# Performance work log

Hardware: AMD Instinct MI355X
Metric: run time of the kernel (lower is better)

The kernel has to match this reference:

```python
import jax, jax.numpy as jnp
import numpy as np

NUM_HEADS = 12

def setup_inputs() -> dict:
    key = jax.random.key(0)
    k1, k2, k3 = jax.random.split(key, 3)
    B, T, H = 2, 2048, 768
    x = jax.random.normal(k1, (B, T, H), dtype=jnp.float32)
    attn_mask = jnp.ones((B, T), dtype=jnp.int32)
    Wqkv = jax.random.normal(k2, (H, 3 * H), dtype=jnp.float32) * 0.02
    bqkv = jnp.zeros((3 * H,), dtype=jnp.float32)
    Wproj = jax.random.normal(k3, (H, H), dtype=jnp.float32) * 0.02
    bproj = jnp.zeros((H,), dtype=jnp.float32)
    return {"x": x, "attn_mask": attn_mask, "Wqkv": Wqkv, "bqkv": bqkv,
            "Wproj": Wproj, "bproj": bproj}

def reference(x, attn_mask, Wqkv, bqkv, Wproj, bproj):
    B, T, H = x.shape
    nh = NUM_HEADS
    hd = H // nh
    qkv = x @ Wqkv + bqkv                      # [B,T,3H]
    q, k, v = jnp.split(qkv, 3, axis=-1)
    # [B,T,H] -> [B,nh,T,hd]
    def heads(t):
        return t.reshape(B, T, nh, hd).transpose(0, 2, 1, 3)
    q, k, v = heads(q), heads(k), heads(v)
    scores = jnp.einsum('bhqd,bhkd->bhqk', q, k) / jnp.sqrt(jnp.float32(hd))
    causal = jnp.tril(jnp.ones((T, T), dtype=bool))          # allowed positions
    key_ok = attn_mask.astype(bool)[:, None, None, :]        # [B,1,1,T]
    allowed = causal[None, None] & key_ok
    scores = jnp.where(allowed, scores, -jnp.inf)
    weights = jax.nn.softmax(scores, axis=-1)                # dropout=0 (eval)
    out = jnp.einsum('bhqk,bhkd->bhqd', weights, v)
    out = out.transpose(0, 2, 1, 3).reshape(B, T, H)
    return out @ Wproj + bproj
```

## Files before the change

kernel.cpp:

```cpp
#include <hip/hip_runtime.h>
#include <stdint.h>

typedef unsigned short u16;
typedef unsigned int   u32;
typedef unsigned char  u8;
typedef __attribute__((ext_vector_type(8))) short short8;
typedef __attribute__((ext_vector_type(4))) float f32x4;
typedef __attribute__((ext_vector_type(4))) unsigned short u16x4;
typedef __attribute__((ext_vector_type(4))) unsigned int u32x4;

#define DEV static __device__ __forceinline__

static constexpr int Bc = 2, Tc = 2048, Hc = 768, NH = 12, HD = 64;
static constexpr int BTc = Bc * Tc;
static constexpr int N3 = 3 * Hc;
static constexpr int NBH = Bc * NH;
static constexpr int NITEMS = 32 * NBH;
static constexpr float QSCALE = 0.125f * 1.44269504088896f;
static constexpr float MRINIT = -1.0e38f;
static constexpr float SMASK  = -3.0e38f;

DEV u16 f2bf(float f) {
  u32 u = __float_as_uint(f);
  u32 r = (u + 0x7fffu + ((u >> 16) & 1u)) >> 16;
  return (u16)r;
}

DEV float fexp2(float x) {
#if __has_builtin(__builtin_amdgcn_exp2f)
  return __builtin_amdgcn_exp2f(x);
#else
  return exp2f(x);
#endif
}

DEV u32 cvtpk_bf16(float lo, float hi) {
  u32 r;
  asm("v_cvt_pk_bf16_f32 %0, %1, %2" : "=v"(r) : "v"(lo), "v"(hi));
  return r;
}

DEV void gl_lds16(const u16* g, u16* l) {
  __builtin_amdgcn_global_load_lds(
      (const __attribute__((address_space(1))) u32*)g,
      (__attribute__((address_space(3))) u32*)l, 16, 0, 0);
}

#define MFMA(a, b, c) __builtin_amdgcn_mfma_f32_16x16x32_bf16((a), (b), (c), 0, 0, 0)

__global__ void k_cvt(const float4* __restrict__ in, uint4* __restrict__ out, int n8,
                      const int* __restrict__ mask, u8* __restrict__ flags,
                      u32* __restrict__ ctr) {
  if (blockIdx.x == 0 && threadIdx.x < 64) {
    int t = threadIdx.x;
    if (t == 0) *ctr = 0;
    int b = t >> 5, kb = t & 31;
    const int* m = mask + b * Tc + kb * 64;
    int all = 1;
    for (int i = 0; i < 64; ++i) all &= (m[i] != 0);
    flags[b * 32 + kb] = (u8)all;
  }
  int i = blockIdx.x * 256 + threadIdx.x;
  if (i >= n8) return;
  float4 a = in[2 * i], b = in[2 * i + 1];
  uint4 o;
  o.x = f2bf(a.x) | ((u32)f2bf(a.y) << 16);
  o.y = f2bf(a.z) | ((u32)f2bf(a.w) << 16);
  o.z = f2bf(b.x) | ((u32)f2bf(b.y) << 16);
  o.w = f2bf(b.z) | ((u32)f2bf(b.w) << 16);
  out[i] = o;
}

__global__ __launch_bounds__(256) void k_transpose_w2(const float* __restrict__ Wqkv,
                                                      const float* __restrict__ Wproj,
                                                      u16* __restrict__ WqkvT,
                                                      u16* __restrict__ WprojT) {
  __shared__ u16 tile[64][65];
  int y = blockIdx.y, x = blockIdx.x;
  const float* in; u16* out; int R, C, r0, c0;
  if (y < 12) { in = Wqkv; out = WqkvT; R = Hc; C = N3; r0 = y * 64; c0 = x * 64; }
  else {
    if (x >= 12) return;
    in = Wproj; out = WprojT; R = Hc; C = Hc; r0 = (y - 12) * 64; c0 = x * 64;
  }
  int tx = threadIdx.x, ty = threadIdx.y;
  for (int i = ty; i < 64; i += 4)
    tile[i][tx] = f2bf(in[(size_t)(r0 + i) * C + c0 + tx]);
  __syncthreads();
  for (int i = ty; i < 64; i += 4)
    out[(size_t)(c0 + i) * R + r0 + tx] = tile[tx][i];
}

template <int EPI>
__global__ __launch_bounds__(256) void k_gemm(const u16* __restrict__ A,
                                              const u16* __restrict__ BTm,
                                              const float* __restrict__ bias,
                                              u16* __restrict__ oQ, u16* __restrict__ oK,
                                              u16* __restrict__ oV, float* __restrict__ oF,
                                              int M, int N, int K) {
  __shared__ u16 As[3][4096];
  __shared__ u16 Bs[3][4096];
  const int tid = threadIdx.x;
  const int lane = tid & 63, wave = tid >> 6;
  const int wr = wave >> 1, wc = wave & 1;

  const int gx = gridDim.x;
  const int nwg = gx * gridDim.y;
  const int lin = blockIdx.y * gx + blockIdx.x;
  const int wg = (lin & 7) * (nwg >> 3) + (lin >> 3);
  const int row0 = (wg / gx) * 128, col0 = (wg % gx) * 128;

  f32x4 acc[4][4];
#pragma unroll
  for (int m = 0; m < 4; ++m)
#pragma unroll
    for (int n = 0; n < 4; ++n) acc[m][n] = (f32x4)(0.f);

  const int srow = lane >> 2;
  const int sg = lane & 3;
  const int sf = (lane >> 3) & 3;
  const int kfetch = ((sg ^ sf) * 8);

  const int r16 = lane & 15;
  const int g = lane >> 4;
  const int fr = (r16 >> 1) & 3;
  const int koff = ((g ^ fr) * 8);

  auto stageG = [&](int slot, int k0) {
#pragma unroll
    for (int p = 0; p < 2; ++p) {
      int seg = wave * 2 + p;
      int row = seg * 16 + srow;
      gl_lds16(A + (size_t)(row0 + row) * K + k0 + kfetch, &As[slot][seg * 512 + lane * 8]);
      gl_lds16(BTm + (size_t)(col0 + row) * K + k0 + kfetch, &Bs[slot][seg * 512 + lane * 8]);
    }
  };

  const int nk = K >> 5;
  stageG(0, 0);
  if (nk > 1) stageG(1, 32);

  for (int kt = 0; kt < nk; ++kt) {
    if (kt + 1 < nk) asm volatile("s_waitcnt vmcnt(4)" ::: "memory");
    else             asm volatile("s_waitcnt vmcnt(0)" ::: "memory");
    __builtin_amdgcn_sched_barrier(0);
    __builtin_amdgcn_s_barrier();
    __builtin_amdgcn_sched_barrier(0);
    if (kt + 2 < nk) stageG((kt + 2) % 3, (kt + 2) * 32);

    const u16* Ac = &As[kt % 3][0];
    const u16* Bcur = &Bs[kt % 3][0];
    short8 af[4], bf[4];
#pragma unroll
    for (int m = 0; m < 4; ++m)
      af[m] = *(const short8*)&Ac[(wr * 64 + m * 16 + r16) * 32 + koff];
#pragma unroll
    for (int n = 0; n < 4; ++n)
      bf[n] = *(const short8*)&Bcur[(wc * 64 + n * 16 + r16) * 32 + koff];
#pragma unroll
    for (int m = 0; m < 4; ++m)
#pragma unroll
      for (int n = 0; n < 4; ++n)
        acc[m][n] = MFMA(af[m], bf[n], acc[m][n]);
  }

#pragma unroll
  for (int m = 0; m < 4; ++m) {
    int rowg = row0 + wr * 64 + m * 16 + g * 4;
#pragma unroll
    for (int n = 0; n < 4; ++n) {
      int colg = col0 + wc * 64 + n * 16 + r16;
      float bv = bias[colg];
      if constexpr (EPI == 0) {
        int which = colg / Hc;
        int hc = colg - which * Hc;
        int h = hc >> 6, d = hc & 63;
        int b = rowg >> 11, t0 = rowg & 2047;
        if (which == 2) {
          int o = t0 & 31;
          int t0p = (t0 & ~31) | (((o >> 2) & 3) * 8 + ((o >> 4) & 1) * 4);
          u16x4 pk;
#pragma unroll
          for (int r = 0; r < 4; ++r) pk[r] = f2bf(acc[m][n][r] + bv);
          *(u16x4*)&oV[((size_t)(b * NH + h) * HD + d) * Tc + t0p] = pk;
        } else {
#pragma unroll
          for (int r = 0; r < 4; ++r) {
            float v = acc[m][n][r] + bv;
            size_t dst = ((size_t)(b * NH + h) * Tc + t0 + r) * HD + d;
            if (which == 0) oQ[dst] = f2bf(v * QSCALE);
            else            oK[dst] = f2bf(v);
          }
        }
      } else {
#pragma unroll
        for (int r = 0; r < 4; ++r)
          oF[(size_t)(rowg + r) * Hc + colg] = acc[m][n][r] + bv;
      }
    }
  }
}

__global__ __launch_bounds__(512, 4) void k_attn(const u16* __restrict__ Qh,
                                                 const u16* __restrict__ Kh,
                                                 const u16* __restrict__ VT,
                                                 const int* __restrict__ mask,
                                                 const u8* __restrict__ flags,
                                                 u16* __restrict__ O,
                                                 u32* __restrict__ ctr) {
  __shared__ u16 Ks[2][4096];
  __shared__ u16 Vs[2][4096];
  __shared__ float mlb[128];
  __shared__ int s_item;
  const int tid = threadIdx.x, lane = tid & 63, wave = tid >> 6;
  const int qgrp = wave >> 1;
  const int kh = wave & 1;
  const int r16 = lane & 15, g = lane >> 4;
  const int r7 = r16 & 7;
  const int skey = lane >> 3;
  const int sgr = lane & 7;
  const int sgd = ((sgr ^ skey) * 8);

  const int off0 = r16 * 64 + ((g ^ r7) * 8);
  const int off1 = r16 * 64 + (((4 + g) ^ r7) * 8);
  const int offv = kh ? off1 : off0;

  for (;;) {
    if (tid == 0) s_item = (int)atomicAdd(ctr, 1u);
    __syncthreads();
    const int item = s_item;
    if (item >= NITEMS) break;
    const int qt = 31 - item / NBH;
    const int bh = item % NBH;
    const int b = bh / NH, h = bh - b * NH;
    const int q0 = qt * 64;
    const int nt = qt + 1;
    const int qg = q0 + qgrp * 16 + r16;
    const int* mrow = mask + b * Tc;
    const u8* frow = flags + b * 32;

    const u16* qbase = Qh + ((size_t)bh * Tc + qg) * HD;
    const short8 qf0 = *(const short8*)(qbase + g * 8);
    const short8 qf1 = *(const short8*)(qbase + 32 + g * 8);

    f32x4 acc[4];
#pragma unroll
    for (int n = 0; n < 4; ++n) acc[n] = (f32x4)(0.f);
    float mrun = MRINIT, lrun = 0.f;

    const u16* kgb = Kh + (size_t)bh * Tc * HD;
    const u16* vgb = VT + (size_t)bh * HD * Tc;

    auto stage = [&](int slot, int kb) {
      int rloc = wave * 8 + skey;
      gl_lds16(kgb + (size_t)(kb + rloc) * HD + sgd, &Ks[slot][wave * 512 + lane * 8]);
      gl_lds16(vgb + (size_t)rloc * Tc + kb + sgd, &Vs[slot][wave * 512 + lane * 8]);
    };

    stage(0, 0);

    for (int t = 0; t < nt; ++t) {
      const int kb = t * 64;

      asm volatile("s_waitcnt vmcnt(0)" ::: "memory");
      __builtin_amdgcn_sched_barrier(0);
      __builtin_amdgcn_s_barrier();
      __builtin_amdgcn_sched_barrier(0);

      if (t + 1 < nt) stage((t + 1) & 1, kb + 64);

      const u16* Kc = &Ks[t & 1][0];
      const u16* Vc = &Vs[t & 1][0];

      f32x4 s0, s1;
      {
        const int ng = 2 * kh;
        short8 kf0 = *(const short8*)&Kc[ng * 1024 + off0];
        short8 kf1 = *(const short8*)&Kc[ng * 1024 + off1];
        f32x4 z = (f32x4)(0.f);
        z = MFMA(kf0, qf0, z); z = MFMA(kf1, qf1, z);
        s0 = z;
        short8 kf2 = *(const short8*)&Kc[(ng + 1) * 1024 + off0];
        short8 kf3 = *(const short8*)&Kc[(ng + 1) * 1024 + off1];
        f32x4 w = (f32x4)(0.f);
        w = MFMA(kf2, qf0, w); w = MFMA(kf3, qf1, w);
        s1 = w;
      }

      const int kbw = kb + 32 * kh;
      const bool diag = (t == nt - 1);
      if (diag || !frow[t]) {
        const int fl = frow[t];
#pragma unroll
        for (int np = 0; np < 2; ++np)
#pragma unroll
          for (int r = 0; r < 4; ++r) {
            int keyg = kbw + 16 * np + 4 * g + r;
            bool ok = fl ? true : (mrow[keyg] != 0);
            if (diag) ok = ok && (keyg <= qg);
            if (!ok) { if (np == 0) s0[r] = SMASK; else s1[r] = SMASK; }
          }
      }

      float lm = fmaxf(fmaxf(fmaxf(s0[0], s0[1]), fmaxf(s0[2], s0[3])),
                       fmaxf(fmaxf(s1[0], s1[1]), fmaxf(s1[2], s1[3])));
      if (!__all(lm <= mrun + 8.0f)) {
        float rm = fmaxf(lm, __shfl_xor(lm, 16));
        rm = fmaxf(rm, __shfl_xor(rm, 32));
        float nm = fmaxf(mrun, rm);
        float alpha = fexp2(mrun - nm);
        mrun = nm;
        lrun *= alpha;
#pragma unroll
        for (int r = 0; r < 4; ++r) {
          float ar = __shfl(alpha, g * 4 + r);
          acc[0][r] *= ar; acc[1][r] *= ar; acc[2][r] *= ar; acc[3][r] *= ar;
        }
      }
      float p0[4], p1[4];
#pragma unroll
      for (int r = 0; r < 4; ++r) {
        p0[r] = fexp2(s0[r] - mrun);
        p1[r] = fexp2(s1[r] - mrun);
      }
      lrun += ((p0[0] + p0[1]) + (p0[2] + p0[3])) + ((p1[0] + p1[1]) + (p1[2] + p1[3]));

      u32x4 PL;
      PL[0] = cvtpk_bf16(p0[0], p0[1]); PL[1] = cvtpk_bf16(p0[2], p0[3]);
      PL[2] = cvtpk_bf16(p1[0], p1[1]); PL[3] = cvtpk_bf16(p1[2], p1[3]);
      short8 pa = __builtin_bit_cast(short8, PL);
#pragma unroll
      for (int n = 0; n < 4; ++n) {
        short8 vf = *(const short8*)&Vc[n * 1024 + offv];
        acc[n] = MFMA(pa, vf, acc[n]);
      }
      __builtin_amdgcn_sched_barrier(0);
    }

    float lt = lrun + __shfl_xor(lrun, 16);
    lt += __shfl_xor(lt, 32);

    __syncthreads();
    float* ab = (float*)&Ks[0][0] + qgrp * 1024;
    if (kh == 1) {
#pragma unroll
      for (int n = 0; n < 4; ++n)
#pragma unroll
        for (int r = 0; r < 4; ++r)
          ab[(4 * g + r) * 64 + 16 * n + r16] = acc[n][r];
      if (g == 0) {
        mlb[qgrp * 32 + r16 * 2]     = mrun;
        mlb[qgrp * 32 + r16 * 2 + 1] = lt;
      }
    }
    __syncthreads();
    if (kh == 0) {
#pragma unroll
      for (int r = 0; r < 4; ++r) {
        int q = 4 * g + r;
        float mA = __shfl(mrun, q);
        float lA = __shfl(lt, q);
        float mB = mlb[qgrp * 32 + q * 2];
        float lB = mlb[qgrp * 32 + q * 2 + 1];
        float ms = fmaxf(mA, mB);
        float cA = fexp2(mA - ms);
        float cB = fexp2(mB - ms);
        float linv = 1.0f / (lA * cA + lB * cB);
        int qr = q0 + qgrp * 16 + q;
        u16* orow = O + ((size_t)(b * Tc + qr)) * Hc + h * 64;
#pragma unroll
        for (int n = 0; n < 4; ++n) {
          float v = (acc[n][r] * cA + ab[q * 64 + 16 * n + r16] * cB) * linv;
          orow[n * 16 + r16] = f2bf(v);
        }
      }
    }
  }
}

extern "C" void kernel_launch(void* const* d_in, const int* in_sizes, int n_in,
                              void* d_out, int out_size, void* d_ws, size_t ws_size,
                              hipStream_t stream) {
  const float* x = (const float*)d_in[0];
  const int* mask = (const int*)d_in[1];
  const float* Wqkv = (const float*)d_in[2];
  const float* bqkv = (const float*)d_in[3];
  const float* Wproj = (const float*)d_in[4];
  const float* bproj = (const float*)d_in[5];
  float* out = (float*)d_out;

  char* ws = (char*)d_ws;
  size_t off = 0;
  auto alloc = [&](size_t bytes) {
    char* p = ws + off;
    off += (bytes + 255) & ~(size_t)255;
    return p;
  };
  u16* xb     = (u16*)alloc((size_t)BTc * Hc * 2);
  u16* WqkvT  = (u16*)alloc((size_t)N3 * Hc * 2);
  u16* WprojT = (u16*)alloc((size_t)Hc * Hc * 2);
  u16* Qh     = (u16*)alloc((size_t)BTc * Hc * 2);
  u16* Kh     = (u16*)alloc((size_t)BTc * Hc * 2);
  u16* VT     = (u16*)alloc((size_t)BTc * Hc * 2);
  u32* ctr    = (u32*)alloc(256);
  u8*  flags  = (u8*)alloc(256);
  u16* Ob     = xb;

  int n8 = BTc * Hc / 8;
  k_cvt<<<(n8 + 255) / 256, 256, 0, stream>>>((const float4*)x, (uint4*)xb, n8,
                                              mask, flags, ctr);
  k_transpose_w2<<<dim3(36, 24), dim3(64, 4), 0, stream>>>(Wqkv, Wproj, WqkvT, WprojT);
  k_gemm<0><<<dim3(N3 / 128, BTc / 128), 256, 0, stream>>>(xb, WqkvT, bqkv, Qh, Kh, VT,
                                                           nullptr, BTc, N3, Hc);
  k_attn<<<dim3(NITEMS), 512, 0, stream>>>(Qh, Kh, VT, mask, flags, Ob, ctr);
  k_gemm<1><<<dim3(Hc / 128, BTc / 128), 256, 0, stream>>>(Ob, WprojT, bproj, nullptr,
                                                           nullptr, nullptr, out, BTc, Hc, Hc);
}
```

Before: 106.7 us.

## Load K/V fragments directly from global, partition attention work per XCD, merge prep kernels

The attention kernel stops staging K and V tiles into LDS through a double-buffered global-to-LDS pipeline with barriers. Each wave now reads its MFMA fragments straight from global memory and relies on cache reuse. Work items are split into per-XCD queues, each with its own atomic counter and three batch-head pairs, so a head's K/V stays in one XCD's L2. The kernel adds s_setprio around the MFMA sections, and the launch is cut to 512 persistent blocks. The cast and transpose prep kernels are merged into one launch. The change risks exposing global-load latency and uncoalesced reads in exchange for removing per-tile barriers.

```diff
diff --git a/kernel.cpp b/kernel.cpp
--- a/kernel.cpp
+++ b/kernel.cpp
@@ -15,7 +15,7 @@
 static constexpr int BTc = Bc * Tc;
 static constexpr int N3 = 3 * Hc;
 static constexpr int NBH = Bc * NH;
-static constexpr int NITEMS = 32 * NBH;
+static constexpr int IPX = 96;
 static constexpr float QSCALE = 0.125f * 1.44269504088896f;
 static constexpr float MRINIT = -1.0e38f;
 static constexpr float SMASK  = -3.0e38f;
@@ -48,47 +48,51 @@
 
 #define MFMA(a, b, c) __builtin_amdgcn_mfma_f32_16x16x32_bf16((a), (b), (c), 0, 0, 0)
 
-__global__ void k_cvt(const float4* __restrict__ in, uint4* __restrict__ out, int n8,
-                      const int* __restrict__ mask, u8* __restrict__ flags,
-                      u32* __restrict__ ctr) {
-  if (blockIdx.x == 0 && threadIdx.x < 64) {
-    int t = threadIdx.x;
-    if (t == 0) *ctr = 0;
-    int b = t >> 5, kb = t & 31;
+__global__ __launch_bounds__(256) void k_prep(const float* __restrict__ x,
+                                              const float* __restrict__ Wqkv,
+                                              const float* __restrict__ Wproj,
+                                              u16* __restrict__ xb,
+                                              u16* __restrict__ WqkvT,
+                                              u16* __restrict__ WprojT,
+                                              const int* __restrict__ mask,
+                                              u8* __restrict__ flags,
+                                              u32* __restrict__ ctr) {
+  const int bid = blockIdx.x, tid = threadIdx.x;
+  if (bid == 0 && tid < 64) {
+    if (tid < 8) ctr[tid] = 0;
+    int b = tid >> 5, kb = tid & 31;
     const int* m = mask + b * Tc + kb * 64;
     int all = 1;
     for (int i = 0; i < 64; ++i) all &= (m[i] != 0);
     flags[b * 32 + kb] = (u8)all;
   }
-  int i = blockIdx.x * 256 + threadIdx.x;
-  if (i >= n8) return;
-  float4 a = in[2 * i], b = in[2 * i + 1];
-  uint4 o;
-  o.x = f2bf(a.x) | ((u32)f2bf(a.y) << 16);
-  o.y = f2bf(a.z) | ((u32)f2bf(a.w) << 16);
-  o.z = f2bf(b.x) | ((u32)f2bf(b.y) << 16);
-  o.w = f2bf(b.z) | ((u32)f2bf(b.w) << 16);
-  out[i] = o;
-}
-
-__global__ __launch_bounds__(256) void k_transpose_w2(const float* __restrict__ Wqkv,
-                                                      const float* __restrict__ Wproj,
-                                                      u16* __restrict__ WqkvT,
-                                                      u16* __restrict__ WprojT) {
-  __shared__ u16 tile[64][65];
-  int y = blockIdx.y, x = blockIdx.x;
-  const float* in; u16* out; int R, C, r0, c0;
-  if (y < 12) { in = Wqkv; out = WqkvT; R = Hc; C = N3; r0 = y * 64; c0 = x * 64; }
-  else {
-    if (x >= 12) return;
-    in = Wproj; out = WprojT; R = Hc; C = Hc; r0 = (y - 12) * 64; c0 = x * 64;
+  if (bid < 864) {
+    __shared__ u16 tile[64][65];
+    int xg = bid % 36, y = bid / 36;
+    const float* in; u16* out; int R, C, r0, c0;
+    if (y < 12) { in = Wqkv; out = WqkvT; R = Hc; C = N3; r0 = y * 64; c0 = xg * 64; }
+    else {
+      if (xg >= 12) return;
+      in = Wproj; out = WprojT; R = Hc; C = Hc; r0 = (y - 12) * 64; c0 = xg * 64;
+    }
+    int tx = tid & 63, ty = tid >> 6;
+    for (int i = ty; i < 64; i += 4)
+      tile[i][tx] = f2bf(in[(size_t)(r0 + i) * C + c0 + tx]);
+    __syncthreads();
+    for (int i = ty; i < 64; i += 4)
+      out[(size_t)(c0 + i) * R + r0 + tx] = tile[tx][i];
+  } else {
+    int i = (bid - 864) * 256 + tid;
+    if (i >= BTc * Hc / 8) return;
+    const float4* in4 = (const float4*)x;
+    float4 a = in4[2 * i], b = in4[2 * i + 1];
+    uint4 o;
+    o.x = f2bf(a.x) | ((u32)f2bf(a.y) << 16);
+    o.y = f2bf(a.z) | ((u32)f2bf(a.w) << 16);
+    o.z = f2bf(b.x) | ((u32)f2bf(b.y) << 16);
+    o.w = f2bf(b.z) | ((u32)f2bf(b.w) << 16);
+    ((uint4*)xb)[i] = o;
   }
-  int tx = threadIdx.x, ty = threadIdx.y;
-  for (int i = ty; i < 64; i += 4)
-    tile[i][tx] = f2bf(in[(size_t)(r0 + i) * C + c0 + tx]);
-  __syncthreads();
-  for (int i = ty; i < 64; i += 4)
-    out[(size_t)(c0 + i) * R + r0 + tx] = tile[tx][i];
 }
 
 template <int EPI>
@@ -208,30 +212,23 @@
                                                  const u8* __restrict__ flags,
                                                  u16* __restrict__ O,
                                                  u32* __restrict__ ctr) {
-  __shared__ u16 Ks[2][4096];
-  __shared__ u16 Vs[2][4096];
+  __shared__ float ab[4][1024];
   __shared__ float mlb[128];
   __shared__ int s_item;
   const int tid = threadIdx.x, lane = tid & 63, wave = tid >> 6;
   const int qgrp = wave >> 1;
   const int kh = wave & 1;
   const int r16 = lane & 15, g = lane >> 4;
-  const int r7 = r16 & 7;
-  const int skey = lane >> 3;
-  const int sgr = lane & 7;
-  const int sgd = ((sgr ^ skey) * 8);
-
-  const int off0 = r16 * 64 + ((g ^ r7) * 8);
-  const int off1 = r16 * 64 + (((4 + g) ^ r7) * 8);
-  const int offv = kh ? off1 : off0;
+
+  const int xcd = blockIdx.x & 7;
 
   for (;;) {
-    if (tid == 0) s_item = (int)atomicAdd(ctr, 1u);
+    if (tid == 0) s_item = (int)atomicAdd(ctr + xcd, 1u);
     __syncthreads();
     const int item = s_item;
-    if (item >= NITEMS) break;
-    const int qt = 31 - item / NBH;
-    const int bh = item % NBH;
+    if (item >= IPX) break;
+    const int qt = 31 - item / 3;
+    const int bh = xcd * 3 + item % 3;
     const int b = bh / NH, h = bh - b * NH;
     const int q0 = qt * 64;
     const int nt = qt + 1;
@@ -248,46 +245,31 @@
     for (int n = 0; n < 4; ++n) acc[n] = (f32x4)(0.f);
     float mrun = MRINIT, lrun = 0.f;
 
-    const u16* kgb = Kh + (size_t)bh * Tc * HD;
-    const u16* vgb = VT + (size_t)bh * HD * Tc;
-
-    auto stage = [&](int slot, int kb) {
-      int rloc = wave * 8 + skey;
-      gl_lds16(kgb + (size_t)(kb + rloc) * HD + sgd, &Ks[slot][wave * 512 + lane * 8]);
-      gl_lds16(vgb + (size_t)rloc * Tc + kb + sgd, &Vs[slot][wave * 512 + lane * 8]);
-    };
-
-    stage(0, 0);
+    const u16* kp = Kh + (size_t)bh * Tc * HD + (size_t)(32 * kh + r16) * HD + 8 * g;
+    const u16* vp = VT + (size_t)bh * HD * Tc + (size_t)r16 * Tc + 32 * kh + 8 * g;
 
     for (int t = 0; t < nt; ++t) {
       const int kb = t * 64;
-
-      asm volatile("s_waitcnt vmcnt(0)" ::: "memory");
-      __builtin_amdgcn_sched_barrier(0);
-      __builtin_amdgcn_s_barrier();
-      __builtin_amdgcn_sched_barrier(0);
-
-      if (t + 1 < nt) stage((t + 1) & 1, kb + 64);
-
-      const u16* Kc = &Ks[t & 1][0];
-      const u16* Vc = &Vs[t & 1][0];
+      const int kbw = kb + 32 * kh;
+
+      const u16* kt0 = kp + (size_t)kb * HD;
+      short8 kf0 = *(const short8*)(kt0);
+      short8 kf1 = *(const short8*)(kt0 + 32);
+      short8 kf2 = *(const short8*)(kt0 + 1024);
+      short8 kf3 = *(const short8*)(kt0 + 1024 + 32);
 
       f32x4 s0, s1;
+      __builtin_amdgcn_s_setprio(1);
       {
-        const int ng = 2 * kh;
-        short8 kf0 = *(const short8*)&Kc[ng * 1024 + off0];
-        short8 kf1 = *(const short8*)&Kc[ng * 1024 + off1];
         f32x4 z = (f32x4)(0.f);
         z = MFMA(kf0, qf0, z); z = MFMA(kf1, qf1, z);
         s0 = z;
-        short8 kf2 = *(const short8*)&Kc[(ng + 1) * 1024 + off0];
-        short8 kf3 = *(const short8*)&Kc[(ng + 1) * 1024 + off1];
         f32x4 w = (f32x4)(0.f);
         w = MFMA(kf2, qf0, w); w = MFMA(kf3, qf1, w);
         s1 = w;
       }
-
-      const int kbw = kb + 32 * kh;
+      __builtin_amdgcn_s_setprio(0);
+
       const bool diag = (t == nt - 1);
       if (diag || !frow[t]) {
         const int fl = frow[t];
@@ -329,25 +311,27 @@
       PL[0] = cvtpk_bf16(p0[0], p0[1]); PL[1] = cvtpk_bf16(p0[2], p0[3]);
       PL[2] = cvtpk_bf16(p1[0], p1[1]); PL[3] = cvtpk_bf16(p1[2], p1[3]);
       short8 pa = __builtin_bit_cast(short8, PL);
+
+      const u16* vt0 = vp + kb;
+      __builtin_amdgcn_s_setprio(1);
 #pragma unroll
       for (int n = 0; n < 4; ++n) {
-        short8 vf = *(const short8*)&Vc[n * 1024 + offv];
+        short8 vf = *(const short8*)(vt0 + (size_t)n * 16 * Tc);
         acc[n] = MFMA(pa, vf, acc[n]);
       }
-      __builtin_amdgcn_sched_barrier(0);
+      __builtin_amdgcn_s_setprio(0);
     }
 
     float lt = lrun + __shfl_xor(lrun, 16);
     lt += __shfl_xor(lt, 32);
 
     __syncthreads();
-    float* ab = (float*)&Ks[0][0] + qgrp * 1024;
     if (kh == 1) {
 #pragma unroll
       for (int n = 0; n < 4; ++n)
 #pragma unroll
         for (int r = 0; r < 4; ++r)
-          ab[(4 * g + r) * 64 + 16 * n + r16] = acc[n][r];
+          ab[qgrp][(4 * g + r) * 64 + 16 * n + r16] = acc[n][r];
       if (g == 0) {
         mlb[qgrp * 32 + r16 * 2]     = mrun;
         mlb[qgrp * 32 + r16 * 2 + 1] = lt;
@@ -370,7 +354,7 @@
         u16* orow = O + ((size_t)(b * Tc + qr)) * Hc + h * 64;
 #pragma unroll
         for (int n = 0; n < 4; ++n) {
-          float v = (acc[n][r] * cA + ab[q * 64 + 16 * n + r16] * cB) * linv;
+          float v = (acc[n][r] * cA + ab[qgrp][q * 64 + 16 * n + r16] * cB) * linv;
           orow[n * 16 + r16] = f2bf(v);
         }
       }
@@ -406,13 +390,11 @@
   u8*  flags  = (u8*)alloc(256);
   u16* Ob     = xb;
 
-  int n8 = BTc * Hc / 8;
-  k_cvt<<<(n8 + 255) / 256, 256, 0, stream>>>((const float4*)x, (uint4*)xb, n8,
-                                              mask, flags, ctr);
-  k_transpose_w2<<<dim3(36, 24), dim3(64, 4), 0, stream>>>(Wqkv, Wproj, WqkvT, WprojT);
+  k_prep<<<dim3(864 + BTc * Hc / 8 / 256), 256, 0, stream>>>(
+      x, Wqkv, Wproj, xb, WqkvT, WprojT, mask, flags, ctr);
   k_gemm<0><<<dim3(N3 / 128, BTc / 128), 256, 0, stream>>>(xb, WqkvT, bqkv, Qh, Kh, VT,
                                                            nullptr, BTc, N3, Hc);
-  k_attn<<<dim3(NITEMS), 512, 0, stream>>>(Qh, Kh, VT, mask, flags, Ob, ctr);
+  k_attn<<<dim3(512), 512, 0, stream>>>(Qh, Kh, VT, mask, flags, Ob, ctr);
   k_gemm<1><<<dim3(Hc / 128, BTc / 128), 256, 0, stream>>>(Ob, WprojT, bproj, nullptr,
                                                            nullptr, nullptr, out, BTc, Hc, Hc);
 }
```

New measurement: 166.2 us. 1.56x slower.
